# Kernel optimization log

Hardware: AMD Instinct MI355X
Metric: run time of the kernel (lower is better)

Reference implementation:

```python
import jax, jax.numpy as jnp
import numpy as np
from jax import lax

L = 5          # integration steps
B, H, W = 8, 256, 256
HID = 100      # res_block hidden channels
KS = 15        # gaussian kernel size
SIGMA = 4.0
MU = 0.02
SLOPE = 0.01   # LeakyReLU default slope


def setup_inputs() -> dict:
    key = jax.random.key(0)
    ks = jax.random.split(key, 7)
    source = jax.random.uniform(ks[0], (B, 1, H, W), jnp.float32)
    target = jax.random.uniform(ks[1], (B, 1, H, W), jnp.float32)
    source_seg = jax.random.uniform(ks[2], (B, 1, H, W), jnp.float32)
    z0 = jax.random.normal(ks[3], (1, 1, H, W), jnp.float32) * 0.01
    w1 = jax.random.normal(ks[4], (L, HID, 3, 3, 3), jnp.float32) / np.sqrt(3 * 9)
    w2 = jax.random.normal(ks[5], (L, HID, HID, 3, 3), jnp.float32) / np.sqrt(HID * 9)
    w3 = jax.random.normal(ks[6], (L, 1, HID, 3, 3), jnp.float32) / np.sqrt(HID * 9)
    return dict(source=source, target=target, source_seg=source_seg, z0=z0, w1=w1, w2=w2, w3=w3)


def _conv(x, w):
    return lax.conv_general_dilated(x, w, (1, 1), [(1, 1), (1, 1)],
                                    dimension_numbers=('NCHW', 'OIHW', 'NCHW'))


def _sobel(img):
    # kornia SpatialGradient(mode='sobel'), normalized kernel (/8), replicate padding
    kx = jnp.array([[-1., 0., 1.], [-2., 0., 2.], [-1., 0., 1.]], jnp.float32) / 8.0
    k = jnp.stack([kx, kx.T])[:, None]  # [2,1,3,3]: (dx, dy)
    xp = jnp.pad(img, ((0, 0), (0, 0), (1, 1), (1, 1)), mode='edge')
    return lax.conv_general_dilated(xp, k, (1, 1), 'VALID',
                                    dimension_numbers=('NCHW', 'OIHW', 'NCHW'))  # [B,2,H,W]


def _gauss1d():
    x = jnp.arange(KS, dtype=jnp.float32) - (KS - 1) / 2.0
    g = jnp.exp(-x * x / (2.0 * SIGMA * SIGMA))
    return g / g.sum()


def _gblur(x):
    # GaussianBlur2d, border_type='constant' (zero pad), separable
    b, c, h, w = x.shape
    g = _gauss1d()
    p = KS // 2
    xr = x.reshape(b * c, 1, h, w)
    xr = jnp.pad(xr, ((0, 0), (0, 0), (p, p), (0, 0)))
    xr = lax.conv_general_dilated(xr, g.reshape(1, 1, KS, 1), (1, 1), 'VALID',
                                  dimension_numbers=('NCHW', 'OIHW', 'NCHW'))
    xr = jnp.pad(xr, ((0, 0), (0, 0), (0, 0), (p, p)))
    xr = lax.conv_general_dilated(xr, g.reshape(1, 1, 1, KS), (1, 1), 'VALID',
                                  dimension_numbers=('NCHW', 'OIHW', 'NCHW'))
    return xr.reshape(b, c, h, w)


def _warp(img, grid):
    # bilinear grid_sample at absolute pixel coords, zeros outside (padding_mode='zeros')
    bc, c, hh, ww = img.shape
    x = grid[..., 0]
    y = grid[..., 1]
    x0 = jnp.floor(x)
    y0 = jnp.floor(y)
    x1 = x0 + 1.0
    y1 = y0 + 1.0

    def corner(xi, yi, wgt):
        inb = ((xi >= 0) & (xi <= ww - 1) & (yi >= 0) & (yi <= hh - 1)).astype(img.dtype)
        xc = jnp.clip(xi, 0, ww - 1).astype(jnp.int32)
        yc = jnp.clip(yi, 0, hh - 1).astype(jnp.int32)
        v = jax.vmap(lambda im, yy, xx: im[:, yy, xx])(img, yc, xc)  # [B,C,H,W]
        return v * (wgt * inb)[:, None, :, :]

    return (corner(x0, y0, (x1 - x) * (y1 - y)) + corner(x1, y0, (x - x0) * (y1 - y)) +
            corner(x0, y1, (x1 - x) * (y - y0)) + corner(x1, y1, (x - x0) * (y - y0)))


def _res_block(z, I, J, w1, w2, w3):
    # dropout is inference-mode identity
    x = jnp.concatenate([z, I, J], axis=1)
    x = jax.nn.leaky_relu(_conv(x, w1), SLOPE)
    x = jax.nn.leaky_relu(_conv(x, w2), SLOPE)
    return _conv(x, w3)


def _forward(source, target, z0, w1, w2, w3):
    bc = source.shape[0]
    gx, gy = jnp.meshgrid(jnp.arange(W, dtype=jnp.float32), jnp.arange(H, dtype=jnp.float32))
    id_grid = jnp.stack([gx, gy], axis=-1)[None]  # [1,H,W,2] pixel coords (x,y)

    image = source
    residuals = [jnp.broadcast_to(z0, (bc, 1, H, W)).astype(source.dtype)]
    fields, grads, phi_list = [], [], []
    for i in range(L):
        g = _sobel(image)                                  # [B,2,H,W]
        grads.append(g)
        field = _gblur(-residuals[i] * g).transpose(0, 2, 3, 1)  # [B,H,W,2]
        fields.append(field)
        deformation = id_grid - field / L                  # [B,H,W,2]
        f = _res_block(residuals[i], image, target, w1[i], w2[i], w3[i]) / L
        residuals.append(residuals[i] - f)
        if i != 0:
            phi_list = [_warp(p.transpose(0, 3, 1, 2), deformation).transpose(0, 2, 3, 1)
                        for p in phi_list]
        phi_list.append(deformation)
        rs = residuals[-1]
        for k in range(len(residuals) - 2):
            rs = rs + _warp(residuals[k + 1], phi_list[k + 1])
        image = _warp(source, phi_list[0]) + rs * (MU * MU) / L
    return image, jnp.stack(fields), jnp.stack(residuals), jnp.stack(grads)


def reference(source, target, source_seg, z0, w1, w2, w3):
    # source_seg is unused in the original forward
    return _forward(source, target, z0, w1, w2, w3)
```

## Files before the change

### kernel.cpp

```cpp
#include <hip/hip_runtime.h>
#include <math.h>

typedef __attribute__((ext_vector_type(8))) short short8;
typedef __attribute__((ext_vector_type(4))) float f32x4;
typedef unsigned int uint;
typedef unsigned short ushort;

#define Lsteps 5
#define Hn 256
#define Wn 256
#define HWn 65536
#define BHW 524288

#define OUT_IMG    0
#define OUT_FIELDS 524288
#define OUT_RES    5767168
#define OUT_GRADS  8912896

#define WS_IMG   0
#define WS_PHIA  524288
#define WS_PHIB  5767168
#define WS_VTMP  11010048
#define WS_W2B   12058624
#define WS_W3P   12381184
#define WS_X2    12386944

__device__ inline float lrelu(float s) { return s > 0.f ? s : 0.01f * s; }

__device__ inline ushort bf16r(float f) {
  uint u = __float_as_uint(f);
  return (ushort)((u + 0x7fffu + ((u >> 16) & 1u)) >> 16);
}

__device__ inline void make_gauss(float* G) {
  float s = 0.f;
#pragma unroll
  for (int t = 0; t < 15; t++) {
    float d = (float)t - 7.f;
    G[t] = expf(-d * d * (1.f / 32.f));
    s += G[t];
  }
  float inv = 1.f / s;
#pragma unroll
  for (int t = 0; t < 15; t++) G[t] *= inv;
}

__device__ inline float bilin1(const float* __restrict__ p, float x, float y) {
  float x0f = floorf(x), y0f = floorf(y);
  int x0 = (int)x0f, y0 = (int)y0f;
  float fx = x - x0f, fy = y - y0f;
  float w00 = (1.f - fx) * (1.f - fy), w10 = fx * (1.f - fy);
  float w01 = (1.f - fx) * fy, w11 = fx * fy;
  float acc = 0.f;
  if ((unsigned)x0 < 256u && (unsigned)y0 < 256u) acc += w00 * p[y0 * 256 + x0];
  if ((unsigned)(x0 + 1) < 256u && (unsigned)y0 < 256u) acc += w10 * p[y0 * 256 + x0 + 1];
  if ((unsigned)x0 < 256u && (unsigned)(y0 + 1) < 256u) acc += w01 * p[(y0 + 1) * 256 + x0];
  if ((unsigned)(x0 + 1) < 256u && (unsigned)(y0 + 1) < 256u) acc += w11 * p[(y0 + 1) * 256 + x0 + 1];
  return acc;
}

__device__ inline void bilin2(const float* __restrict__ p, float x, float y,
                              float& o0, float& o1) {
  float x0f = floorf(x), y0f = floorf(y);
  int x0 = (int)x0f, y0 = (int)y0f;
  float fx = x - x0f, fy = y - y0f;
  float w00 = (1.f - fx) * (1.f - fy), w10 = fx * (1.f - fy);
  float w01 = (1.f - fx) * fy, w11 = fx * fy;
  o0 = 0.f; o1 = 0.f;
  if ((unsigned)x0 < 256u && (unsigned)y0 < 256u) {
    const float* q = p + (y0 * 256 + x0) * 2; o0 += w00 * q[0]; o1 += w00 * q[1];
  }
  if ((unsigned)(x0 + 1) < 256u && (unsigned)y0 < 256u) {
    const float* q = p + (y0 * 256 + x0 + 1) * 2; o0 += w10 * q[0]; o1 += w10 * q[1];
  }
  if ((unsigned)x0 < 256u && (unsigned)(y0 + 1) < 256u) {
    const float* q = p + ((y0 + 1) * 256 + x0) * 2; o0 += w01 * q[0]; o1 += w01 * q[1];
  }
  if ((unsigned)(x0 + 1) < 256u && (unsigned)(y0 + 1) < 256u) {
    const float* q = p + ((y0 + 1) * 256 + x0 + 1) * 2; o0 += w11 * q[0]; o1 += w11 * q[1];
  }
}

__global__ void init_res0_kernel(const float* __restrict__ z0, float* __restrict__ res0) {
  int idx = blockIdx.x * 256 + threadIdx.x;
  res0[idx] = z0[idx & 65535];
}

__global__ void w2b_prep(const float* __restrict__ w2, ushort* __restrict__ w2b) {
  int idx = blockIdx.x * 256 + threadIdx.x;
  if (idx >= Lsteps * 129024) return;
  int l = idx / 129024;
  int r = idx - l * 129024;
  int tap = r / 14336;
  int r2 = r - tap * 14336;
  int kc = r2 / 3584;
  int r3 = r2 - kc * 3584;
  int o = r3 >> 9;
  int r4 = r3 & 511;
  int lane = r4 >> 3;
  int j = r4 & 7;
  int q = lane >> 4, n = lane & 15;
  int oc = o * 16 + n;
  int ic = (kc < 3 ? kc * 32 : 72) + q * 8 + j;
  bool real = (oc < 100) && (kc < 3 ? true : (ic >= 96 && ic < 100));
  float v = real ? w2[l * 90000 + oc * 900 + ic * 9 + tap] : 0.f;
  w2b[idx] = bf16r(v);
}

__global__ void w3p_prep(const float* __restrict__ w3, float* __restrict__ w3p) {
  int idx = blockIdx.x * 256 + threadIdx.x;
  if (idx >= Lsteps * 9 * 128) return;
  int l = idx / 1152;
  int r = idx - l * 1152;
  int tap = r >> 7;
  int ic = r & 127;
  w3p[idx] = (ic < 100) ? w3[l * 900 + ic * 9 + tap] : 0.f;
}

__global__ __launch_bounds__(256) void field_fused(
    const float* __restrict__ img, const float* __restrict__ res_i,
    float* __restrict__ grads_i, float* __restrict__ fields_i) {
  __shared__ float sBuf[2560];
  __shared__ float sP[2][2400];
  const int tid = threadIdx.x;
  const int b = blockIdx.z;
  const int Y0 = blockIdx.y * 16, X0 = blockIdx.x * 64;
  float G[15]; make_gauss(G);
  const float* ib = img + b * HWn;
  const float* rb = res_i + b * HWn;

  for (int u = tid; u < 2560; u += 256) {
    int ly = u / 80, lx = u - ly * 80;
    int gy = Y0 - 8 + ly, gx = X0 - 8 + lx;
    gy = gy < 0 ? 0 : (gy > 255 ? 255 : gy);
    gx = gx < 0 ? 0 : (gx > 255 ? 255 : gx);
    sBuf[u] = ib[gy * 256 + gx];
  }
  __syncthreads();

  for (int u = tid; u < 2400; u += 256) {
    int ly = u / 80, lx = u - ly * 80;
    int gy = Y0 - 7 + ly, gx = X0 - 7 + lx;
    float p0 = 0.f, p1 = 0.f;
    if (lx < 78 && (unsigned)gy < 256u && (unsigned)gx < 256u) {
      int base = (ly + 1) * 80 + (lx + 1);
      float a00 = sBuf[base - 81], a01 = sBuf[base - 80], a02 = sBuf[base - 79];
      float a10 = sBuf[base - 1], a12 = sBuf[base + 1];
      float a20 = sBuf[base + 79], a21 = sBuf[base + 80], a22 = sBuf[base + 81];
      float gxs = (a02 - a00 + 2.f * (a12 - a10) + a22 - a20) * 0.125f;
      float gys = (a20 - a00 + 2.f * (a21 - a01) + a22 - a02) * 0.125f;
      float r = rb[gy * 256 + gx];
      p0 = -r * gxs; p1 = -r * gys;
      if (ly >= 7 && ly < 23 && lx >= 7 && lx < 71) {
        grads_i[b * 131072 + gy * 256 + gx] = gxs;
        grads_i[b * 131072 + 65536 + gy * 256 + gx] = gys;
      }
    }
    sP[0][u] = p0; sP[1][u] = p1;
  }
  __syncthreads();

  for (int u = tid; u < 2560; u += 256) {
    int c = u >= 1280 ? 1 : 0;
    int v = u - c * 1280;
    int ly = v / 80, lx = v - ly * 80;
    float s = 0.f;
    if (lx < 78) {
      const float* pc = &sP[c][ly * 80 + lx];
#pragma unroll
      for (int t = 0; t < 15; t++) s += G[t] * pc[t * 80];
    }
    sBuf[u] = s;
  }
  __syncthreads();

  for (int u = tid; u < 2048; u += 256) {
    int c = u >> 10, v = u & 1023;
    int ly = v >> 6, lx = v & 63;
    const float* tc = sBuf + c * 1280 + ly * 80 + lx;
    float s = 0.f;
#pragma unroll
    for (int t = 0; t < 15; t++) s += G[t] * tc[t];
    int gy = Y0 + ly, gx = X0 + lx;
    fields_i[(b * 65536 + gy * 256 + gx) * 2 + c] = s;
  }
}

__global__ __launch_bounds__(256, 4) void conv12_kernel(
    const float* __restrict__ res_i, const float* __restrict__ img,
    const float* __restrict__ tgt, const float* __restrict__ w1,
    const short8* __restrict__ w2b, ushort* __restrict__ x2) {
  __shared__ ushort x1s[180 * 104];
  const int tid = threadIdx.x;
  const int b = blockIdx.z;
  const int Y0 = blockIdx.y * 8, X0 = blockIdx.x * 16;
  const float* zb = res_i + b * HWn;
  const float* ib = img + b * HWn;
  const float* tb = tgt + b * HWn;

  if (tid < 180) {
    int ly = tid / 18, lx = tid - ly * 18;
    int gy = Y0 + ly - 1, gx = X0 + lx - 1;
    const bool inb = (unsigned)gy < 256u && (unsigned)gx < 256u;
    float p[27];
#pragma unroll
    for (int dy = 0; dy < 3; dy++)
#pragma unroll
      for (int dx = 0; dx < 3; dx++) {
        int yy = gy + dy - 1, xx = gx + dx - 1;
        bool ok = (unsigned)yy < 256u && (unsigned)xx < 256u;
        int o = ok ? (yy * 256 + xx) : 0;
        int j = dy * 3 + dx;
        p[j] = ok ? zb[o] : 0.f;
        p[9 + j] = ok ? ib[o] : 0.f;
        p[18 + j] = ok ? tb[o] : 0.f;
      }
    const uint base = (uint)tid * 104u;
    for (int oc = 0; oc < 100; oc += 2) {
      const float* wa = w1 + oc * 27;
      float s0 = 0.f, s1 = 0.f;
#pragma unroll
      for (int j = 0; j < 27; j++) {
        s0 = fmaf(p[j], wa[j], s0);
        s1 = fmaf(p[j], wa[27 + j], s1);
      }
      s0 = inb ? lrelu(s0) : 0.f;
      s1 = inb ? lrelu(s1) : 0.f;
      *(uint*)&x1s[base + oc] = (uint)bf16r(s0) | ((uint)bf16r(s1) << 16);
    }
    *(uint*)&x1s[base + 100] = 0u;
    *(uint*)&x1s[base + 102] = 0u;
  }
  __syncthreads();

  const int lane = tid & 63, wv = tid >> 6;
  const int q = lane >> 4, n = lane & 15;
  f32x4 acc[8][2];
#pragma unroll
  for (int r = 0; r < 8; r++)
#pragma unroll
    for (int f = 0; f < 2; f++) acc[r][f] = (f32x4)(0.f);

  const short8* wsrc = w2b + lane + (uint)(wv * 2) * 64u;
  auto loadw = [&](short8 (&dst)[2], int it) {
    const short8* s = wsrc + (it >> 2) * 1792 + (it & 3) * 448;
    dst[0] = s[0];
    dst[1] = s[64];
  };
  auto compute = [&](short8 (&w)[2], int it) {
    const int tap = it >> 2, kc = it & 3;
    const int dy = tap / 3, dx = tap - dy * 3;
    const int koff = (kc < 3 ? kc * 32 : 72) + q * 8;
    const uint abase = (uint)(dy * 18 + n + dx) * 104u + (uint)koff;
    __builtin_amdgcn_s_setprio(1);
#pragma unroll
    for (int r = 0; r < 8; r++) {
      short8 a = *(const short8*)&x1s[abase + (uint)r * 1872u];
      acc[r][0] = __builtin_amdgcn_mfma_f32_16x16x32_bf16(a, w[0], acc[r][0], 0, 0, 0);
      acc[r][1] = __builtin_amdgcn_mfma_f32_16x16x32_bf16(a, w[1], acc[r][1], 0, 0, 0);
    }
    __builtin_amdgcn_s_setprio(0);
  };

  short8 wA[2], wB[2];
  loadw(wA, 0);
#pragma unroll
  for (int it = 0; it < 36; it += 2) {
    loadw(wB, it + 1);
    compute(wA, it);
    if (it + 2 < 36) loadw(wA, it + 2);
    compute(wB, it + 1);
  }

  __syncthreads();
#pragma unroll
  for (int f = 0; f < 2; f++) {
    const int o = wv * 2 + f;
    if (o < 7) {
      const int oc = o * 16 + n;
      if (oc < 104) {
#pragma unroll
        for (int r = 0; r < 8; r++) {
#pragma unroll
          for (int v = 0; v < 4; v++) {
            const int pix = r * 16 + q * 4 + v;
            x1s[pix * 104 + oc] = bf16r(lrelu(acc[r][f][v]));
          }
        }
      }
    }
  }
  __syncthreads();
  ushort* xg = x2 + (size_t)((b << 16) + Y0 * 256 + X0) * 104;
  for (int u = tid; u < 1664; u += 256) {
    int pix = u / 13, ch = u - pix * 13;
    int y = pix >> 4, x = pix & 15;
    uint4 val = *(const uint4*)&x1s[pix * 104 + ch * 8];
    *(uint4*)(xg + (size_t)(y * 256 + x) * 104 + ch * 8) = val;
  }
}

__global__ __launch_bounds__(256, 2) void cpi_fused(
    const float* __restrict__ res_i,
    const ushort* __restrict__ x2,
    const float* __restrict__ w3p,
    const float* __restrict__ fields_i,
    const float* __restrict__ phi_src,
    float* __restrict__ phi_dst,
    const float* __restrict__ source,
    const float* __restrict__ res_base,
    float* __restrict__ res_n,
    float* __restrict__ img_out, int step) {
  __shared__ ushort sx[324 * 104];
  const int tid = threadIdx.x;
  const int b = blockIdx.z;
  const int Y0 = blockIdx.y * 16, X0 = blockIdx.x * 16;

  for (int u = tid; u < 4212; u += 256) {
    int pix = u / 13, ch = u - pix * 13;
    int py = pix / 18, px = pix - py * 18;
    int gy = Y0 - 1 + py, gx = X0 - 1 + px;
    uint4 v = make_uint4(0u, 0u, 0u, 0u);
    if ((unsigned)gy < 256u && (unsigned)gx < 256u)
      v = *(const uint4*)(x2 + (size_t)((b << 16) + gy * 256 + gx) * 104 + ch * 8);
    *(uint4*)&sx[pix * 104 + ch * 8] = v;
  }
  __syncthreads();

  const int ly = tid >> 4, lx = tid & 15;
  const int y = Y0 + ly, x = X0 + lx;
  const int idx = (b << 16) + y * 256 + x;

  float acc = 0.f;
#pragma unroll
  for (int tap = 0; tap < 9; tap++) {
    int dy = tap / 3, dx = tap - dy * 3;
    const ushort* px_ = &sx[((ly + dy) * 18 + (lx + dx)) * 104];
    const float* wt = w3p + tap * 128;
#pragma unroll
    for (int c = 0; c < 13; c++) {
      uint4 u = *(const uint4*)(px_ + c * 8);
      const float* w8 = wt + c * 8;
      acc = fmaf(__uint_as_float(u.x << 16), w8[0], acc);
      acc = fmaf(__uint_as_float(u.x & 0xffff0000u), w8[1], acc);
      acc = fmaf(__uint_as_float(u.y << 16), w8[2], acc);
      acc = fmaf(__uint_as_float(u.y & 0xffff0000u), w8[3], acc);
      acc = fmaf(__uint_as_float(u.z << 16), w8[4], acc);
      acc = fmaf(__uint_as_float(u.z & 0xffff0000u), w8[5], acc);
      acc = fmaf(__uint_as_float(u.w << 16), w8[6], acc);
      acc = fmaf(__uint_as_float(u.w & 0xffff0000u), w8[7], acc);
    }
  }
  float rn = res_i[idx] - 0.2f * acc;
  res_n[idx] = rn;

  int pix2 = (y * 256 + x) * 2;
  float f0 = fields_i[2 * idx], f1 = fields_i[2 * idx + 1];
  float dxp = (float)x - f0 * 0.2f;
  float dyp = (float)y - f1 * 0.2f;
  float img = 0.f, rs = rn;
  for (int k = 0; k <= step; k++) {
    float o0, o1;
    if (k == step) { o0 = dxp; o1 = dyp; }
    else bilin2(phi_src + (size_t)(k * 8 + b) * 131072, dxp, dyp, o0, o1);
    float* dst = phi_dst + (size_t)(k * 8 + b) * 131072 + pix2;
    dst[0] = o0; dst[1] = o1;
    if (k == 0) img = bilin1(source + b * HWn, o0, o1);
    else rs += bilin1(res_base + (size_t)k * BHW + b * HWn, o0, o1);
  }
  img_out[idx] = img + rs * 8.0e-5f;
}

extern "C" void kernel_launch(void* const* d_in, const int* in_sizes, int n_in,
                              void* d_out, int out_size, void* d_ws, size_t ws_size,
                              hipStream_t stream) {
  const float* source = (const float*)d_in[0];
  const float* target = (const float*)d_in[1];
  const float* z0 = (const float*)d_in[3];
  const float* w1 = (const float*)d_in[4];
  const float* w2 = (const float*)d_in[5];
  const float* w3 = (const float*)d_in[6];
  float* out = (float*)d_out;
  float* ws = (float*)d_ws;

  float* ws_img = ws + WS_IMG;
  float* phiA = ws + WS_PHIA;
  float* phiB = ws + WS_PHIB;
  ushort* w2b = (ushort*)(ws + WS_W2B);
  float* w3p = ws + WS_W3P;
  ushort* x2 = (ushort*)(ws + WS_X2);

  hipMemcpyAsync(ws_img, source, BHW * sizeof(float), hipMemcpyDeviceToDevice, stream);
  init_res0_kernel<<<BHW / 256, 256, 0, stream>>>(z0, out + OUT_RES);
  w2b_prep<<<(Lsteps * 129024 + 255) / 256, 256, 0, stream>>>(w2, w2b);
  w3p_prep<<<23, 256, 0, stream>>>(w3, w3p);

  for (int i = 0; i < Lsteps; i++) {
    float* grads_i = out + OUT_GRADS + (size_t)i * 1048576;
    float* fields_i = out + OUT_FIELDS + (size_t)i * 1048576;
    const float* res_i = out + OUT_RES + (size_t)i * BHW;
    float* res_n = out + OUT_RES + (size_t)(i + 1) * BHW;
    float* phi_dst = (i % 2 == 0) ? phiA : phiB;
    float* phi_src = (i % 2 == 0) ? phiB : phiA;

    field_fused<<<dim3(4, 16, 8), 256, 0, stream>>>(ws_img, res_i, grads_i, fields_i);
    conv12_kernel<<<dim3(16, 32, 8), 256, 0, stream>>>(
        res_i, ws_img, target, w1 + i * 2700,
        (const short8*)(w2b + (size_t)i * 129024), x2);
    cpi_fused<<<dim3(16, 16, 8), 256, 0, stream>>>(
        res_i, x2, w3p + i * 1152, fields_i, phi_src, phi_dst,
        source, out + OUT_RES, res_n, ws_img, i);
  }
  hipMemcpyAsync(out + OUT_IMG, ws_img, BHW * sizeof(float), hipMemcpyDeviceToDevice, stream);
}
```

Baseline: 1.452 ms.

## Reuse LDS A-fragments across dy taps in conv12 and split cpi kernel

The conv2 MFMA loop is reordered to go kc→dx→dy. For each (kc,dx) it loads 10 row fragments from LDS into registers and reuses them for all three dy taps, so LDS reads drop from 24 to 10 per group, at the cost of more registers. Occupancy is lowered from 4 to 3 to make room for them. Separately, the fused conv3/warp kernel is split into a conv3-residual kernel and a flat per-pixel phi/image warp kernel. This may relieve register pressure in the conv3 kernel but adds a launch and a round trip of res_n through global memory.

Result: faster. 1.422 ms (-2.1%).

```diff
diff --git a/kernel.cpp b/kernel.cpp
--- a/kernel.cpp
+++ b/kernel.cpp
@@ -186,7 +186,7 @@
   }
 }
 
-__global__ __launch_bounds__(256, 4) void conv12_kernel(
+__global__ __launch_bounds__(256, 3) void conv12_kernel(
     const float* __restrict__ res_i, const float* __restrict__ img,
     const float* __restrict__ tgt, const float* __restrict__ w1,
     const short8* __restrict__ w2b, ushort* __restrict__ x2) {
@@ -242,34 +242,39 @@
     for (int f = 0; f < 2; f++) acc[r][f] = (f32x4)(0.f);
 
   const short8* wsrc = w2b + lane + (uint)(wv * 2) * 64u;
-  auto loadw = [&](short8 (&dst)[2], int it) {
-    const short8* s = wsrc + (it >> 2) * 1792 + (it & 3) * 448;
-    dst[0] = s[0];
-    dst[1] = s[64];
+  short8 wbuf[2][2];
+  auto loadw = [&](int slot, int m) {
+    const int kcw = m / 9, rm = m - kcw * 9;
+    const int dxw = rm / 3, dyw = rm - dxw * 3;
+    const short8* s = wsrc + (dyw * 3 + dxw) * 1792 + kcw * 448;
+    wbuf[slot][0] = s[0];
+    wbuf[slot][1] = s[64];
   };
-  auto compute = [&](short8 (&w)[2], int it) {
-    const int tap = it >> 2, kc = it & 3;
-    const int dy = tap / 3, dx = tap - dy * 3;
+  loadw(0, 0);
+
+#pragma unroll
+  for (int kc = 0; kc < 4; kc++) {
     const int koff = (kc < 3 ? kc * 32 : 72) + q * 8;
-    const uint abase = (uint)(dy * 18 + n + dx) * 104u + (uint)koff;
-    __builtin_amdgcn_s_setprio(1);
-#pragma unroll
-    for (int r = 0; r < 8; r++) {
-      short8 a = *(const short8*)&x1s[abase + (uint)r * 1872u];
-      acc[r][0] = __builtin_amdgcn_mfma_f32_16x16x32_bf16(a, w[0], acc[r][0], 0, 0, 0);
-      acc[r][1] = __builtin_amdgcn_mfma_f32_16x16x32_bf16(a, w[1], acc[r][1], 0, 0, 0);
-    }
-    __builtin_amdgcn_s_setprio(0);
-  };
-
-  short8 wA[2], wB[2];
-  loadw(wA, 0);
-#pragma unroll
-  for (int it = 0; it < 36; it += 2) {
-    loadw(wB, it + 1);
-    compute(wA, it);
-    if (it + 2 < 36) loadw(wA, it + 2);
-    compute(wB, it + 1);
+#pragma unroll
+    for (int dx = 0; dx < 3; dx++) {
+      const uint cb = (uint)(n + dx) * 104u + (uint)koff;
+      short8 Ar[10];
+#pragma unroll
+      for (int rr = 0; rr < 10; rr++)
+        Ar[rr] = *(const short8*)&x1s[cb + (uint)rr * 1872u];
+#pragma unroll
+      for (int dy = 0; dy < 3; dy++) {
+        const int m = kc * 9 + dx * 3 + dy;
+        if (m + 1 < 36) loadw((m + 1) & 1, m + 1);
+        __builtin_amdgcn_s_setprio(1);
+#pragma unroll
+        for (int r = 0; r < 8; r++) {
+          acc[r][0] = __builtin_amdgcn_mfma_f32_16x16x32_bf16(Ar[dy + r], wbuf[m & 1][0], acc[r][0], 0, 0, 0);
+          acc[r][1] = __builtin_amdgcn_mfma_f32_16x16x32_bf16(Ar[dy + r], wbuf[m & 1][1], acc[r][1], 0, 0, 0);
+        }
+        __builtin_amdgcn_s_setprio(0);
+      }
+    }
   }
 
   __syncthreads();
@@ -300,17 +305,11 @@
   }
 }
 
-__global__ __launch_bounds__(256, 2) void cpi_fused(
+__global__ __launch_bounds__(256, 2) void conv3res_kernel(
     const float* __restrict__ res_i,
     const ushort* __restrict__ x2,
     const float* __restrict__ w3p,
-    const float* __restrict__ fields_i,
-    const float* __restrict__ phi_src,
-    float* __restrict__ phi_dst,
-    const float* __restrict__ source,
-    const float* __restrict__ res_base,
-    float* __restrict__ res_n,
-    float* __restrict__ img_out, int step) {
+    float* __restrict__ res_n) {
   __shared__ ushort sx[324 * 104];
   const int tid = threadIdx.x;
   const int b = blockIdx.z;
@@ -351,14 +350,24 @@
       acc = fmaf(__uint_as_float(u.w & 0xffff0000u), w8[7], acc);
     }
   }
-  float rn = res_i[idx] - 0.2f * acc;
-  res_n[idx] = rn;
-
+  res_n[idx] = res_i[idx] - 0.2f * acc;
+}
+
+__global__ __launch_bounds__(256) void phiimg_kernel(
+    const float* __restrict__ fields_i,
+    const float* __restrict__ phi_src,
+    float* __restrict__ phi_dst,
+    const float* __restrict__ source,
+    const float* __restrict__ res_base,
+    const float* __restrict__ res_n,
+    float* __restrict__ img_out, int step) {
+  int idx = blockIdx.x * 256 + threadIdx.x;
+  int b = idx >> 16, y = (idx >> 8) & 255, x = idx & 255;
   int pix2 = (y * 256 + x) * 2;
   float f0 = fields_i[2 * idx], f1 = fields_i[2 * idx + 1];
   float dxp = (float)x - f0 * 0.2f;
   float dyp = (float)y - f1 * 0.2f;
-  float img = 0.f, rs = rn;
+  float img = 0.f, rs = res_n[idx];
   for (int k = 0; k <= step; k++) {
     float o0, o1;
     if (k == step) { o0 = dxp; o1 = dyp; }
@@ -407,9 +416,10 @@
     conv12_kernel<<<dim3(16, 32, 8), 256, 0, stream>>>(
         res_i, ws_img, target, w1 + i * 2700,
         (const short8*)(w2b + (size_t)i * 129024), x2);
-    cpi_fused<<<dim3(16, 16, 8), 256, 0, stream>>>(
-        res_i, x2, w3p + i * 1152, fields_i, phi_src, phi_dst,
-        source, out + OUT_RES, res_n, ws_img, i);
+    conv3res_kernel<<<dim3(16, 16, 8), 256, 0, stream>>>(
+        res_i, x2, w3p + i * 1152, res_n);
+    phiimg_kernel<<<BHW / 256, 256, 0, stream>>>(
+        fields_i, phi_src, phi_dst, source, out + OUT_RES, res_n, ws_img, i);
   }
   hipMemcpyAsync(out + OUT_IMG, ws_img, BHW * sizeof(float), hipMemcpyDeviceToDevice, stream);
 }
```
